# Kernel optimization log

Hardware: AMD Instinct MI355X
Metric: run time of the kernel (lower is better)

Reference implementation:

```python
import jax, jax.numpy as jnp
import numpy as np

TAU = 1.0
NUM_CLASSES = 256
N = 65536
D = 256
EPS = 1e-12  # F.normalize default eps


def _l2_normalize(x):
    norm = jnp.sqrt(jnp.sum(x * x, axis=-1, keepdims=True))
    return x / jnp.maximum(norm, EPS)


def setup_inputs() -> dict:
    key = jax.random.key(0)
    k1, k2, k3 = jax.random.split(key, 3)
    z1 = jax.random.normal(k1, (N, D), dtype=jnp.float32)
    z2 = jax.random.normal(k2, (N, D), dtype=jnp.float32)
    labels = jax.random.randint(k3, (N,), 0, NUM_CLASSES, dtype=jnp.int32)
    return {"z1_features": z1, "z2_features": z2, "labels": labels}


def reference(z1_features, z2_features, labels):
    # labels for both views: [2N]
    labels2 = jnp.concatenate([labels, labels], axis=0)
    z = jnp.concatenate([_l2_normalize(z1_features), _l2_normalize(z2_features)], axis=0)  # [2N, D]

    # per-class mean via segment-sum (replaces the python loop over unique labels)
    sums = jax.ops.segment_sum(z, labels2, num_segments=NUM_CLASSES)            # [C, D]
    counts = jax.ops.segment_sum(jnp.ones((z.shape[0],), z.dtype), labels2,
                                 num_segments=NUM_CLASSES)                       # [C]
    feature_means = sums / jnp.maximum(counts, 1.0)[:, None]                     # [C, D]

    # sim_proto: row-wise dot of each sample with its own class prototype
    # (original wastefully did diag(means_repeated @ z.T))
    proto_per_row = feature_means[labels2]                                        # [2N, D] gather
    sim_proto = jnp.sum(proto_per_row * z, axis=-1) / TAU                         # [2N]

    sim_all = (z @ feature_means.T) / TAU                                         # [2N, C]
    exp_sim = jnp.exp(sim_all - sim_proto[:, None])
    log_prob_pos = sim_proto - jnp.log(jnp.sum(exp_sim, axis=1))
    return -jnp.mean(log_prob_pos)
```

## Files before the change

### kernel.cpp

```cpp
#include <hip/hip_runtime.h>
#include <hip/hip_bf16.h>


constexpr int N_ROWS = 65536;
constexpr int D_DIM  = 256;
constexpr int C_CLS  = 256;
constexpr int TWO_N  = 2 * N_ROWS;
constexpr int BUCKET = 1024;
constexpr float EPS_NORM = 1e-12f;

typedef short          short8   __attribute__((ext_vector_type(8)));
typedef float          f32x16   __attribute__((ext_vector_type(16)));
typedef unsigned short ushort8v __attribute__((ext_vector_type(8)));

constexpr size_t WS_CURSOR = 0;
constexpr size_t WS_LOSSP  = 4096;
constexpr size_t WS_INVN   = 8192;
constexpr size_t WS_ORDER  = WS_INVN + 4ull * TWO_N;
constexpr size_t WS_MEANP  = WS_ORDER + 4ull * C_CLS * BUCKET;
constexpr size_t WS_MEANS  = WS_MEANP + 16ull * C_CLS * D_DIM;

__device__ __forceinline__ void gload_lds16(const void* g, void* l) {
    __builtin_amdgcn_global_load_lds(
        (const __attribute__((address_space(1))) void*)g,
        (__attribute__((address_space(3))) void*)l, 16, 0, 0);
}

__device__ __forceinline__ unsigned short f2bf(float x) {
    __hip_bfloat16 h = __float2bfloat16(x);
    return __builtin_bit_cast(unsigned short, h);
}

__global__ __launch_bounds__(256)
void k_norm(const float* __restrict__ z1, const float* __restrict__ z2,
            float* __restrict__ inv_norm)
{
    const int w = threadIdx.x >> 6, lane = threadIdx.x & 63;
    const int wave = blockIdx.x * 4 + w;
    #pragma unroll 1
    for (int b = 0; b < 4; ++b) {
        int r[4]; float4 v[4]; float s[4];
        #pragma unroll
        for (int j = 0; j < 4; ++j) {
            r[j] = wave + 8192 * (b * 4 + j);
            const float* src = (r[j] < N_ROWS) ? z1 + (size_t)r[j] * D_DIM
                                               : z2 + (size_t)(r[j] - N_ROWS) * D_DIM;
            v[j] = reinterpret_cast<const float4*>(src)[lane];
        }
        #pragma unroll
        for (int j = 0; j < 4; ++j)
            s[j] = v[j].x * v[j].x + v[j].y * v[j].y + v[j].z * v[j].z + v[j].w * v[j].w;
        #pragma unroll
        for (int off = 1; off < 64; off <<= 1) {
            #pragma unroll
            for (int j = 0; j < 4; ++j) s[j] += __shfl_xor(s[j], off, 64);
        }
        if (lane == 0) {
            #pragma unroll
            for (int j = 0; j < 4; ++j)
                inv_norm[r[j]] = 1.0f / fmaxf(sqrtf(s[j]), EPS_NORM);
        }
    }
}

__global__ __launch_bounds__(256)
void k_scatter(const int* __restrict__ labels, int* __restrict__ cursor,
               int* __restrict__ order)
{
    __shared__ int lcur[C_CLS];
    __shared__ int lbase[C_CLS];
    const int t = threadIdx.x;
    lcur[t] = 0;
    __syncthreads();
    const int i0 = blockIdx.x * 2048;
    int lab[8], lpos[8];
    #pragma unroll
    for (int u = 0; u < 8; ++u) {
        const int i = i0 + u * 256 + t;
        lab[u] = labels[(i < N_ROWS) ? i : (i - N_ROWS)];
        lpos[u] = atomicAdd(&lcur[lab[u]], 1);
    }
    __syncthreads();
    if (lcur[t] > 0) lbase[t] = atomicAdd(&cursor[t], lcur[t]);
    __syncthreads();
    #pragma unroll
    for (int u = 0; u < 8; ++u)
        order[lab[u] * BUCKET + lbase[lab[u]] + lpos[u]] = i0 + u * 256 + t;
}

__global__ __launch_bounds__(256)
void k_means(const float* __restrict__ z1, const float* __restrict__ z2,
             const float* __restrict__ inv_norm, const int* __restrict__ cursor,
             const int* __restrict__ order, float* __restrict__ meanp)
{
    __shared__ float4 red4[4][64];
    const int c = blockIdx.x, sgt = blockIdx.y;
    const int lane = threadIdx.x & 63, w = threadIdx.x >> 6;
    const int cnt = cursor[c];
    const int chunk = (cnt + 3) >> 2;
    const int beg = sgt * chunk;
    const int end = min(beg + chunk, cnt);
    const int* ord = order + c * BUCKET;
    float4 acc = {0.f, 0.f, 0.f, 0.f};
    int idx = beg + w;
    for (; idx + 12 < end; idx += 16) {
        int rr[4]; float4 v[4]; float iv[4];
        #pragma unroll
        for (int u = 0; u < 4; ++u) rr[u] = ord[idx + 4 * u];
        #pragma unroll
        for (int u = 0; u < 4; ++u) {
            const float* src = (rr[u] < N_ROWS) ? z1 + (size_t)rr[u] * D_DIM
                                                : z2 + (size_t)(rr[u] - N_ROWS) * D_DIM;
            v[u] = reinterpret_cast<const float4*>(src)[lane];
            iv[u] = inv_norm[rr[u]];
        }
        #pragma unroll
        for (int u = 0; u < 4; ++u) {
            acc.x = fmaf(v[u].x, iv[u], acc.x);
            acc.y = fmaf(v[u].y, iv[u], acc.y);
            acc.z = fmaf(v[u].z, iv[u], acc.z);
            acc.w = fmaf(v[u].w, iv[u], acc.w);
        }
    }
    for (; idx < end; idx += 4) {
        const int r1 = ord[idx];
        const float* src = (r1 < N_ROWS) ? z1 + (size_t)r1 * D_DIM
                                         : z2 + (size_t)(r1 - N_ROWS) * D_DIM;
        const float4 v = reinterpret_cast<const float4*>(src)[lane];
        const float iv = inv_norm[r1];
        acc.x = fmaf(v.x, iv, acc.x); acc.y = fmaf(v.y, iv, acc.y);
        acc.z = fmaf(v.z, iv, acc.z); acc.w = fmaf(v.w, iv, acc.w);
    }
    red4[w][lane] = acc;
    __syncthreads();
    if (w == 0) {
        const float4 a0 = red4[0][lane], a1 = red4[1][lane];
        const float4 a2 = red4[2][lane], a3 = red4[3][lane];
        float4 o;
        o.x = a0.x + a1.x + a2.x + a3.x;  o.y = a0.y + a1.y + a2.y + a3.y;
        o.z = a0.z + a1.z + a2.z + a3.z;  o.w = a0.w + a1.w + a2.w + a3.w;
        *reinterpret_cast<float4*>(meanp + ((size_t)c * 4 + sgt) * D_DIM + 4 * lane) = o;
    }
}

__global__ __launch_bounds__(256)
void k_means2(const float* __restrict__ meanp, const int* __restrict__ cursor,
              __hip_bfloat16* __restrict__ means)
{
    const int tid = blockIdx.x * 256 + threadIdx.x;
    const int c = tid >> 6, l = tid & 63;
    const float invc = 1.0f / fmaxf((float)cursor[c], 1.0f);
    const float4 s0 = *reinterpret_cast<const float4*>(meanp + ((size_t)c * 4 + 0) * D_DIM + 4 * l);
    const float4 s1 = *reinterpret_cast<const float4*>(meanp + ((size_t)c * 4 + 1) * D_DIM + 4 * l);
    const float4 s2 = *reinterpret_cast<const float4*>(meanp + ((size_t)c * 4 + 2) * D_DIM + 4 * l);
    const float4 s3 = *reinterpret_cast<const float4*>(meanp + ((size_t)c * 4 + 3) * D_DIM + 4 * l);
    ushort4 o;
    o.x = f2bf((s0.x + s1.x + s2.x + s3.x) * invc);
    o.y = f2bf((s0.y + s1.y + s2.y + s3.y) * invc);
    o.z = f2bf((s0.z + s1.z + s2.z + s3.z) * invc);
    o.w = f2bf((s0.w + s1.w + s2.w + s3.w) * invc);
    *reinterpret_cast<ushort4*>(means + (size_t)c * D_DIM + 4 * l) = o;
}

__global__ __launch_bounds__(256, 2)
void k_main(const float* __restrict__ z1, const float* __restrict__ z2,
            const float* __restrict__ inv_norm, const int* __restrict__ labels,
            const __hip_bfloat16* __restrict__ means, float* __restrict__ lossp)
{
    __shared__ char smem[65536];
    const int t    = threadIdx.x;
    const int lane = t & 63;
    const int w    = t >> 6;
    const int wr   = w >> 1, wc = w & 1;
    const int l31  = lane & 31;
    const int g16  = (lane >> 5) << 4;
    const int row0 = blockIdx.x * 128;

    const int a_row  = t >> 1;
    const int a_half = t & 1;
    const int grow   = row0 + a_row;
    const float* zsrc = (grow < N_ROWS) ? z1 + (size_t)grow * D_DIM
                                        : z2 + (size_t)(grow - N_ROWS) * D_DIM;
    const float inv_a = inv_norm[grow];
    const int  a_key  = (((a_row & 3) ^ ((a_row >> 3) & 3)) << 4);
    char* const aw0 = smem + a_row * 64 + ((a_half * 32 + 0)  ^ a_key);
    char* const aw1 = smem + a_row * 64 + ((a_half * 32 + 16) ^ a_key);

    const int rkey = (((l31 & 3) ^ ((l31 >> 3) & 3)) << 4);
    f32x16 acc[2][4] = {};
    float4 pre[4];

    auto A_LOAD = [&](int kt) {
        const float4* s = reinterpret_cast<const float4*>(zsrc + kt * 32 + a_half * 16);
        pre[0] = s[0]; pre[1] = s[1]; pre[2] = s[2]; pre[3] = s[3];
    };
    auto A_WRITE = [&](int buf) {
        ushort8v o1, o2;
        o1[0] = f2bf(pre[0].x * inv_a); o1[1] = f2bf(pre[0].y * inv_a);
        o1[2] = f2bf(pre[0].z * inv_a); o1[3] = f2bf(pre[0].w * inv_a);
        o1[4] = f2bf(pre[1].x * inv_a); o1[5] = f2bf(pre[1].y * inv_a);
        o1[6] = f2bf(pre[1].z * inv_a); o1[7] = f2bf(pre[1].w * inv_a);
        o2[0] = f2bf(pre[2].x * inv_a); o2[1] = f2bf(pre[2].y * inv_a);
        o2[2] = f2bf(pre[2].z * inv_a); o2[3] = f2bf(pre[2].w * inv_a);
        o2[4] = f2bf(pre[3].x * inv_a); o2[5] = f2bf(pre[3].y * inv_a);
        o2[6] = f2bf(pre[3].z * inv_a); o2[7] = f2bf(pre[3].w * inv_a);
        *reinterpret_cast<ushort8v*>(aw0 + buf * 8192) = o1;
        *reinterpret_cast<ushort8v*>(aw1 + buf * 8192) = o2;
    };
    auto B_STAGE = [&](int kt, int buf) {
        #pragma unroll
        for (int q = 0; q < 4; ++q) {
            const int g   = q * 256 + t;
            const int c   = g >> 2;
            const int cb  = (g & 3) << 4;
            const int key = (((c & 3) ^ ((c >> 3) & 3)) << 4);
            gload_lds16((const char*)means + (size_t)c * 512 + kt * 64 + (cb ^ key),
                        smem + 16384 + buf * 16384 + q * 4096 + w * 1024);
        }
    };
    auto COMPUTE = [&](int buf) {
        const char* ab = smem + buf * 8192;
        const char* bb = smem + 16384 + buf * 16384;
        #pragma unroll
        for (int ks = 0; ks < 2; ++ks) {
            const int cb = (ks * 32 + g16) ^ rkey;
            const short8 a0 = *reinterpret_cast<const short8*>(ab + (wr * 64 + l31) * 64 + cb);
            const short8 a1 = *reinterpret_cast<const short8*>(ab + (wr * 64 + 32 + l31) * 64 + cb);
            short8 bfr[4];
            #pragma unroll
            for (int n = 0; n < 4; ++n)
                bfr[n] = *reinterpret_cast<const short8*>(bb + (wc * 128 + n * 32 + l31) * 64 + cb);
            #pragma unroll
            for (int n = 0; n < 4; ++n) {
                acc[0][n] = __builtin_amdgcn_mfma_f32_32x32x16_bf16(a0, bfr[n], acc[0][n], 0, 0, 0);
                acc[1][n] = __builtin_amdgcn_mfma_f32_32x32x16_bf16(a1, bfr[n], acc[1][n], 0, 0, 0);
            }
        }
    };

    B_STAGE(0, 0);
    A_LOAD(0);
    A_WRITE(0);
    #pragma unroll
    for (int kt = 0; kt < 8; ++kt) {
        __syncthreads();
        if (kt < 7) { B_STAGE(kt + 1, (kt + 1) & 1); A_LOAD(kt + 1); }
        COMPUTE(kt & 1);
        if (kt < 7) A_WRITE((kt + 1) & 1);
    }
    __syncthreads();

    float* simf = reinterpret_cast<float*>(smem);
    float partial = 0.0f;
    for (int rhalf = 0; rhalf < 2; ++rhalf) {
        if (wr == rhalf) {
            #pragma unroll
            for (int rt = 0; rt < 2; ++rt)
                #pragma unroll
                for (int n = 0; n < 4; ++n)
                    #pragma unroll
                    for (int q = 0; q < 16; ++q) {
                        const int row64 = rt * 32 + (q & 3) + 8 * (q >> 2) + 4 * (lane >> 5);
                        const int col   = wc * 128 + n * 32 + l31;
                        simf[row64 * 256 + col] = acc[rt][n][q];
                    }
        }
        __syncthreads();
        #pragma unroll 1
        for (int i = 0; i < 16; ++i) {
            const int rl    = w * 16 + i;
            const int growr = row0 + rhalf * 64 + rl;
            float s = __expf(simf[rl * 256 + lane])       + __expf(simf[rl * 256 + 64 + lane])
                    + __expf(simf[rl * 256 + 128 + lane]) + __expf(simf[rl * 256 + 192 + lane]);
            #pragma unroll
            for (int off = 32; off; off >>= 1) s += __shfl_down(s, off, 64);
            const int lab = labels[(growr < N_ROWS) ? growr : growr - N_ROWS];
            const float sp = simf[rl * 256 + lab];
            if (lane == 0) partial += 2.0f * sp - logf(s);
        }
        __syncthreads();
    }
    if (lane == 0) simf[w] = partial;
    __syncthreads();
    if (t == 0) lossp[blockIdx.x] = simf[0] + simf[1] + simf[2] + simf[3];
}

__global__ __launch_bounds__(256)
void k_final(const float* __restrict__ lossp, float* __restrict__ out)
{
    __shared__ float red[4];
    const int t = threadIdx.x, lane = t & 63, w = t >> 6;
    float s = lossp[t] + lossp[t + 256] + lossp[t + 512] + lossp[t + 768];
    #pragma unroll
    for (int off = 32; off; off >>= 1) s += __shfl_down(s, off, 64);
    if (lane == 0) red[w] = s;
    __syncthreads();
    if (t == 0) out[0] = -(red[0] + red[1] + red[2] + red[3]) / (float)TWO_N;
}

extern "C" void kernel_launch(void* const* d_in, const int* in_sizes, int n_in,
                              void* d_out, int out_size, void* d_ws, size_t ws_size,
                              hipStream_t stream)
{
    const float* z1     = (const float*)d_in[0];
    const float* z2     = (const float*)d_in[1];
    const int*   labels = (const int*)d_in[2];
    float* out = (float*)d_out;
    char*  ws  = (char*)d_ws;

    int*   cursor   = (int*)  (ws + WS_CURSOR);
    float* lossp    = (float*)(ws + WS_LOSSP);
    float* inv_norm = (float*)(ws + WS_INVN);
    int*   order    = (int*)  (ws + WS_ORDER);
    float* meanp    = (float*)(ws + WS_MEANP);
    __hip_bfloat16* means = (__hip_bfloat16*)(ws + WS_MEANS);

    hipMemsetAsync(ws, 0, 4096, stream);

    hipLaunchKernelGGL(k_norm,    dim3(2048), dim3(256), 0, stream, z1, z2, inv_norm);
    hipLaunchKernelGGL(k_scatter, dim3(64),   dim3(256), 0, stream, labels, cursor, order);
    hipLaunchKernelGGL(k_means,   dim3(256, 4), dim3(256), 0, stream, z1, z2, inv_norm, cursor, order, meanp);
    hipLaunchKernelGGL(k_means2,  dim3(64),   dim3(256), 0, stream, meanp, cursor, means);
    hipLaunchKernelGGL(k_main,    dim3(TWO_N / 128), dim3(256), 0, stream, z1, z2, inv_norm, labels, means, lossp);
    hipLaunchKernelGGL(k_final,   dim3(1),    dim3(256), 0, stream, lossp, out);
}
```

Measured before the change: 236.7 us.

## Materialize normalized bf16 features once and reuse them across means and main kernels

Normalization now writes a bf16 copy of the L2-normalized features, so the class-mean and similarity kernels read half-size data instead of re-reading fp32 inputs and rescaling. The main kernel computes exp-sums and the prototype similarity straight from MFMA accumulators and reduces the loss with an atomic add, which removes the final reduction kernel. This path needs a large workspace and falls back to the old kernels otherwise. Class means are now taken from bf16-rounded features, which slightly changes numerics.

```diff
diff --git a/kernel.cpp b/kernel.cpp
--- a/kernel.cpp
+++ b/kernel.cpp
@@ -13,27 +13,291 @@
 typedef float          f32x16   __attribute__((ext_vector_type(16)));
 typedef unsigned short ushort8v __attribute__((ext_vector_type(8)));
 
-constexpr size_t WS_CURSOR = 0;
-constexpr size_t WS_LOSSP  = 4096;
-constexpr size_t WS_INVN   = 8192;
-constexpr size_t WS_ORDER  = WS_INVN + 4ull * TWO_N;
-constexpr size_t WS_MEANP  = WS_ORDER + 4ull * C_CLS * BUCKET;
-constexpr size_t WS_MEANS  = WS_MEANP + 16ull * C_CLS * D_DIM;
+constexpr size_t CW_CURSOR = 0;
+constexpr size_t CW_MEANP  = 4096;
+constexpr size_t CW_MEANS  = CW_MEANP + 524288;
+constexpr size_t CW_ORDER  = CW_MEANS + 131072;
+constexpr size_t CW_ZNB    = CW_ORDER + 1048576;
+constexpr size_t CW_NEED   = CW_ZNB + 2ull * TWO_N * D_DIM;
+
+constexpr size_t FW_CURSOR = 0;
+constexpr size_t FW_LOSSP  = 4096;
+constexpr size_t FW_INVN   = 8192;
+constexpr size_t FW_ORDER  = FW_INVN + 4ull * TWO_N;
+constexpr size_t FW_MEANP  = FW_ORDER + 4ull * C_CLS * BUCKET;
+constexpr size_t FW_MEANS  = FW_MEANP + 16ull * C_CLS * D_DIM;
 
 __device__ __forceinline__ void gload_lds16(const void* g, void* l) {
     __builtin_amdgcn_global_load_lds(
         (const __attribute__((address_space(1))) void*)g,
         (__attribute__((address_space(3))) void*)l, 16, 0, 0);
 }
-
 __device__ __forceinline__ unsigned short f2bf(float x) {
     __hip_bfloat16 h = __float2bfloat16(x);
     return __builtin_bit_cast(unsigned short, h);
 }
+__device__ __forceinline__ float bf2f(unsigned short u) {
+    return __uint_as_float(((unsigned int)u) << 16);
+}
+
+__global__ __launch_bounds__(256)
+void k_scatter(const int* __restrict__ labels, int* __restrict__ cursor,
+               int* __restrict__ order)
+{
+    __shared__ int lcur[C_CLS];
+    __shared__ int lbase[C_CLS];
+    const int t = threadIdx.x;
+    lcur[t] = 0;
+    __syncthreads();
+    const int i0 = blockIdx.x * 2048;
+    int lab[8], lpos[8];
+    #pragma unroll
+    for (int u = 0; u < 8; ++u) {
+        const int i = i0 + u * 256 + t;
+        lab[u] = labels[(i < N_ROWS) ? i : (i - N_ROWS)];
+        lpos[u] = atomicAdd(&lcur[lab[u]], 1);
+    }
+    __syncthreads();
+    if (lcur[t] > 0) lbase[t] = atomicAdd(&cursor[t], lcur[t]);
+    __syncthreads();
+    #pragma unroll
+    for (int u = 0; u < 8; ++u)
+        order[lab[u] * BUCKET + lbase[lab[u]] + lpos[u]] = i0 + u * 256 + t;
+}
+
 
 __global__ __launch_bounds__(256)
 void k_norm(const float* __restrict__ z1, const float* __restrict__ z2,
-            float* __restrict__ inv_norm)
+            __hip_bfloat16* __restrict__ znb)
+{
+    const int w = threadIdx.x >> 6, lane = threadIdx.x & 63;
+    const int wave = blockIdx.x * 4 + w;
+    #pragma unroll 1
+    for (int b = 0; b < 8; ++b) {
+        const int r0 = wave + 8192 * (2 * b);
+        const int r1 = wave + 8192 * (2 * b + 1);
+        const float* s0p = (r0 < N_ROWS) ? z1 + (size_t)r0 * D_DIM
+                                         : z2 + (size_t)(r0 - N_ROWS) * D_DIM;
+        const float* s1p = (r1 < N_ROWS) ? z1 + (size_t)r1 * D_DIM
+                                         : z2 + (size_t)(r1 - N_ROWS) * D_DIM;
+        const float4 v0 = reinterpret_cast<const float4*>(s0p)[lane];
+        const float4 v1 = reinterpret_cast<const float4*>(s1p)[lane];
+        float s0 = v0.x * v0.x + v0.y * v0.y + v0.z * v0.z + v0.w * v0.w;
+        float s1 = v1.x * v1.x + v1.y * v1.y + v1.z * v1.z + v1.w * v1.w;
+        #pragma unroll
+        for (int off = 1; off < 64; off <<= 1) {
+            s0 += __shfl_xor(s0, off, 64);
+            s1 += __shfl_xor(s1, off, 64);
+        }
+        const float i0 = 1.0f / fmaxf(sqrtf(s0), EPS_NORM);
+        const float i1 = 1.0f / fmaxf(sqrtf(s1), EPS_NORM);
+        ushort4 o0, o1;
+        o0.x = f2bf(v0.x * i0); o0.y = f2bf(v0.y * i0);
+        o0.z = f2bf(v0.z * i0); o0.w = f2bf(v0.w * i0);
+        o1.x = f2bf(v1.x * i1); o1.y = f2bf(v1.y * i1);
+        o1.z = f2bf(v1.z * i1); o1.w = f2bf(v1.w * i1);
+        reinterpret_cast<ushort4*>(znb + (size_t)r0 * D_DIM)[lane] = o0;
+        reinterpret_cast<ushort4*>(znb + (size_t)r1 * D_DIM)[lane] = o1;
+    }
+}
+
+__global__ __launch_bounds__(256)
+void k_meansC(const __hip_bfloat16* __restrict__ znb, const int* __restrict__ cursor,
+              const int* __restrict__ order, float* __restrict__ meanp)
+{
+    __shared__ float red[4][D_DIM];
+    const int c = blockIdx.x, sgt = blockIdx.y;
+    const int t = threadIdx.x, lane = t & 63, w = t >> 6;
+    const int h = lane >> 5, l31 = lane & 31;
+    const int cnt = cursor[c];
+    const int chunk = (cnt + 1) >> 1;
+    const int beg = sgt * chunk;
+    const int end = min(beg + chunk, cnt);
+    const int* ord = order + c * BUCKET;
+
+    float acc[8] = {};
+    int base = beg;
+    for (; base + 32 <= end; base += 32) {
+        #pragma unroll
+        for (int u = 0; u < 4; ++u) {
+            const int r = ord[base + w * 8 + u * 2 + h];
+            const ushort8v v = *reinterpret_cast<const ushort8v*>(
+                znb + (size_t)r * D_DIM + l31 * 8);
+            #pragma unroll
+            for (int j = 0; j < 8; ++j) acc[j] += bf2f(v[j]);
+        }
+    }
+    if (base < end) {
+        #pragma unroll
+        for (int u = 0; u < 4; ++u) {
+            const int ri = base + w * 8 + u * 2 + h;
+            const bool ok = ri < end;
+            const int r = ord[ok ? ri : beg];
+            const ushort8v v = *reinterpret_cast<const ushort8v*>(
+                znb + (size_t)r * D_DIM + l31 * 8);
+            const float sc = ok ? 1.0f : 0.0f;
+            #pragma unroll
+            for (int j = 0; j < 8; ++j) acc[j] += bf2f(v[j]) * sc;
+        }
+    }
+    #pragma unroll
+    for (int j = 0; j < 8; ++j) acc[j] += __shfl_xor(acc[j], 32, 64);
+    if (h == 0) {
+        #pragma unroll
+        for (int j = 0; j < 8; ++j) red[w][l31 * 8 + j] = acc[j];
+    }
+    __syncthreads();
+    const float s = red[0][t] + red[1][t] + red[2][t] + red[3][t];
+    meanp[((size_t)sgt * C_CLS + c) * D_DIM + t] = s;
+}
+
+__global__ __launch_bounds__(256)
+void k_means2C(const float* __restrict__ meanp, const int* __restrict__ cursor,
+               __hip_bfloat16* __restrict__ means)
+{
+    const int tid = blockIdx.x * 256 + threadIdx.x;
+    const int c = tid >> 6, l = tid & 63;
+    const float invc = 1.0f / fmaxf((float)cursor[c], 1.0f);
+    const float4 s0 = *reinterpret_cast<const float4*>(meanp + (size_t)c * D_DIM + 4 * l);
+    const float4 s1 = *reinterpret_cast<const float4*>(meanp + (size_t)(C_CLS + c) * D_DIM + 4 * l);
+    ushort4 o;
+    o.x = f2bf((s0.x + s1.x) * invc);
+    o.y = f2bf((s0.y + s1.y) * invc);
+    o.z = f2bf((s0.z + s1.z) * invc);
+    o.w = f2bf((s0.w + s1.w) * invc);
+    *reinterpret_cast<ushort4*>(means + (size_t)c * D_DIM + 4 * l) = o;
+}
+
+__global__ __launch_bounds__(256, 2)
+void k_mainC(const __hip_bfloat16* __restrict__ znb, const int* __restrict__ labels,
+             const __hip_bfloat16* __restrict__ means, float* __restrict__ out)
+{
+    __shared__ char smem[51712];
+    int*   labs   = reinterpret_cast<int*>(smem + 49152);
+    float* expsum = reinterpret_cast<float*>(smem + 49664);
+    float* proto  = reinterpret_cast<float*>(smem + 50688);
+
+    const int t    = threadIdx.x;
+    const int lane = t & 63;
+    const int w    = t >> 6;
+    const int wr   = w >> 1, wc = w & 1;
+    const int l31  = lane & 31;
+    const int g    = lane >> 5;
+    const int g16  = g << 4;
+    const int row0 = blockIdx.x * 128;
+
+    const char* znbB   = (const char*)znb;
+    const char* meansB = (const char*)means;
+
+    const int skey = ((lane >> 3) & 3) << 4;
+    const int sc   = ((lane & 3) << 4) ^ skey;
+    const int rk   = ((l31 >> 1) & 3) << 4;
+
+    auto A_STAGE = [&](int kt, int buf) {
+        #pragma unroll
+        for (int i = 0; i < 2; ++i) {
+            const int row = w * 32 + i * 16 + (lane >> 2);
+            gload_lds16(znbB + (size_t)(row0 + row) * 512 + kt * 64 + sc,
+                        smem + buf * 8192 + (w * 2 + i) * 1024);
+        }
+    };
+    auto B_STAGE = [&](int kt, int buf) {
+        #pragma unroll
+        for (int j = 0; j < 4; ++j) {
+            const int cls = w * 64 + j * 16 + (lane >> 2);
+            gload_lds16(meansB + (size_t)cls * 512 + kt * 64 + sc,
+                        smem + 16384 + buf * 16384 + (w * 4 + j) * 1024);
+        }
+    };
+
+    f32x16 acc[2][4] = {};
+    auto COMPUTE = [&](int buf) {
+        const char* ab = smem + buf * 8192;
+        const char* bb = smem + 16384 + buf * 16384;
+        #pragma unroll
+        for (int ks = 0; ks < 2; ++ks) {
+            const int co = (ks * 32 + g16) ^ rk;
+            const short8 a0 = *reinterpret_cast<const short8*>(ab + (wr * 64 + l31) * 64 + co);
+            const short8 a1 = *reinterpret_cast<const short8*>(ab + (wr * 64 + 32 + l31) * 64 + co);
+            short8 bfr[4];
+            #pragma unroll
+            for (int n = 0; n < 4; ++n)
+                bfr[n] = *reinterpret_cast<const short8*>(
+                    bb + (wc * 128 + n * 32 + l31) * 64 + co);
+            #pragma unroll
+            for (int n = 0; n < 4; ++n) {
+                acc[0][n] = __builtin_amdgcn_mfma_f32_32x32x16_bf16(a0, bfr[n], acc[0][n], 0, 0, 0);
+                acc[1][n] = __builtin_amdgcn_mfma_f32_32x32x16_bf16(a1, bfr[n], acc[1][n], 0, 0, 0);
+            }
+        }
+    };
+
+    if (t < 128) {
+        const int gr = row0 + t;
+        labs[t] = labels[(gr < N_ROWS) ? gr : gr - N_ROWS];
+    }
+    A_STAGE(0, 0);
+    B_STAGE(0, 0);
+    __syncthreads();
+
+    #pragma unroll
+    for (int kt = 0; kt < 8; ++kt) {
+        if (kt < 7) { A_STAGE(kt + 1, (kt + 1) & 1); B_STAGE(kt + 1, (kt + 1) & 1); }
+        COMPUTE(kt & 1);
+        __syncthreads();
+    }
+
+    float rowsum[2][16];
+    #pragma unroll
+    for (int rt = 0; rt < 2; ++rt)
+        #pragma unroll
+        for (int q = 0; q < 16; ++q) {
+            float s = __expf(acc[rt][0][q]) + __expf(acc[rt][1][q])
+                    + __expf(acc[rt][2][q]) + __expf(acc[rt][3][q]);
+            rowsum[rt][q] = s;
+        }
+    #pragma unroll
+    for (int off = 1; off <= 16; off <<= 1) {
+        #pragma unroll
+        for (int rt = 0; rt < 2; ++rt)
+            #pragma unroll
+            for (int q = 0; q < 16; ++q)
+                rowsum[rt][q] += __shfl_xor(rowsum[rt][q], off, 64);
+    }
+    if (l31 == 0) {
+        #pragma unroll
+        for (int rt = 0; rt < 2; ++rt)
+            #pragma unroll
+            for (int q = 0; q < 16; ++q) {
+                const int r = wr * 64 + rt * 32 + (q & 3) + 8 * (q >> 2) + 4 * g;
+                expsum[r * 2 + wc] = rowsum[rt][q];
+            }
+    }
+    #pragma unroll
+    for (int rt = 0; rt < 2; ++rt)
+        #pragma unroll
+        for (int q = 0; q < 16; ++q) {
+            const int r = wr * 64 + rt * 32 + (q & 3) + 8 * (q >> 2) + 4 * g;
+            const int lab = labs[r];
+            #pragma unroll
+            for (int n = 0; n < 4; ++n)
+                if (lab == wc * 128 + n * 32 + l31) proto[r] = acc[rt][n][q];
+        }
+    __syncthreads();
+
+    if (t < 128) {
+        const float es = expsum[t * 2] + expsum[t * 2 + 1];
+        float lp = 2.0f * proto[t] - __logf(es);
+        #pragma unroll
+        for (int off = 1; off < 64; off <<= 1) lp += __shfl_xor(lp, off, 64);
+        if (lane == 0) atomicAdd(out, -lp * (1.0f / (float)TWO_N));
+    }
+}
+
+
+__global__ __launch_bounds__(256)
+void k_norm_fb(const float* __restrict__ z1, const float* __restrict__ z2,
+               float* __restrict__ inv_norm)
 {
     const int w = threadIdx.x >> 6, lane = threadIdx.x & 63;
     const int wave = blockIdx.x * 4 + w;
@@ -64,34 +328,9 @@
 }
 
 __global__ __launch_bounds__(256)
-void k_scatter(const int* __restrict__ labels, int* __restrict__ cursor,
-               int* __restrict__ order)
-{
-    __shared__ int lcur[C_CLS];
-    __shared__ int lbase[C_CLS];
-    const int t = threadIdx.x;
-    lcur[t] = 0;
-    __syncthreads();
-    const int i0 = blockIdx.x * 2048;
-    int lab[8], lpos[8];
-    #pragma unroll
-    for (int u = 0; u < 8; ++u) {
-        const int i = i0 + u * 256 + t;
-        lab[u] = labels[(i < N_ROWS) ? i : (i - N_ROWS)];
-        lpos[u] = atomicAdd(&lcur[lab[u]], 1);
-    }
-    __syncthreads();
-    if (lcur[t] > 0) lbase[t] = atomicAdd(&cursor[t], lcur[t]);
-    __syncthreads();
-    #pragma unroll
-    for (int u = 0; u < 8; ++u)
-        order[lab[u] * BUCKET + lbase[lab[u]] + lpos[u]] = i0 + u * 256 + t;
-}
-
-__global__ __launch_bounds__(256)
-void k_means(const float* __restrict__ z1, const float* __restrict__ z2,
-             const float* __restrict__ inv_norm, const int* __restrict__ cursor,
-             const int* __restrict__ order, float* __restrict__ meanp)
+void k_means_fb(const float* __restrict__ z1, const float* __restrict__ z2,
+                const float* __restrict__ inv_norm, const int* __restrict__ cursor,
+                const int* __restrict__ order, float* __restrict__ meanp)
 {
     __shared__ float4 red4[4][64];
     const int c = blockIdx.x, sgt = blockIdx.y;
@@ -144,8 +383,8 @@
 }
 
 __global__ __launch_bounds__(256)
-void k_means2(const float* __restrict__ meanp, const int* __restrict__ cursor,
-              __hip_bfloat16* __restrict__ means)
+void k_means2_fb(const float* __restrict__ meanp, const int* __restrict__ cursor,
+                 __hip_bfloat16* __restrict__ means)
 {
     const int tid = blockIdx.x * 256 + threadIdx.x;
     const int c = tid >> 6, l = tid & 63;
@@ -163,9 +402,9 @@
 }
 
 __global__ __launch_bounds__(256, 2)
-void k_main(const float* __restrict__ z1, const float* __restrict__ z2,
-            const float* __restrict__ inv_norm, const int* __restrict__ labels,
-            const __hip_bfloat16* __restrict__ means, float* __restrict__ lossp)
+void k_main_fb(const float* __restrict__ z1, const float* __restrict__ z2,
+               const float* __restrict__ inv_norm, const int* __restrict__ labels,
+               const __hip_bfloat16* __restrict__ means, float* __restrict__ lossp)
 {
     __shared__ char smem[65536];
     const int t    = threadIdx.x;
@@ -210,9 +449,9 @@
     auto B_STAGE = [&](int kt, int buf) {
         #pragma unroll
         for (int q = 0; q < 4; ++q) {
-            const int g   = q * 256 + t;
-            const int c   = g >> 2;
-            const int cb  = (g & 3) << 4;
+            const int gg  = q * 256 + t;
+            const int c   = gg >> 2;
+            const int cb  = (gg & 3) << 4;
             const int key = (((c & 3) ^ ((c >> 3) & 3)) << 4);
             gload_lds16((const char*)means + (size_t)c * 512 + kt * 64 + (cb ^ key),
                         smem + 16384 + buf * 16384 + q * 4096 + w * 1024);
@@ -286,7 +525,7 @@
 }
 
 __global__ __launch_bounds__(256)
-void k_final(const float* __restrict__ lossp, float* __restrict__ out)
+void k_final_fb(const float* __restrict__ lossp, float* __restrict__ out)
 {
     __shared__ float red[4];
     const int t = threadIdx.x, lane = t & 63, w = t >> 6;
@@ -308,19 +547,36 @@
     float* out = (float*)d_out;
     char*  ws  = (char*)d_ws;
 
-    int*   cursor   = (int*)  (ws + WS_CURSOR);
-    float* lossp    = (float*)(ws + WS_LOSSP);
-    float* inv_norm = (float*)(ws + WS_INVN);
-    int*   order    = (int*)  (ws + WS_ORDER);
-    float* meanp    = (float*)(ws + WS_MEANP);
-    __hip_bfloat16* means = (__hip_bfloat16*)(ws + WS_MEANS);
-
-    hipMemsetAsync(ws, 0, 4096, stream);
-
-    hipLaunchKernelGGL(k_norm,    dim3(2048), dim3(256), 0, stream, z1, z2, inv_norm);
-    hipLaunchKernelGGL(k_scatter, dim3(64),   dim3(256), 0, stream, labels, cursor, order);
-    hipLaunchKernelGGL(k_means,   dim3(256, 4), dim3(256), 0, stream, z1, z2, inv_norm, cursor, order, meanp);
-    hipLaunchKernelGGL(k_means2,  dim3(64),   dim3(256), 0, stream, meanp, cursor, means);
-    hipLaunchKernelGGL(k_main,    dim3(TWO_N / 128), dim3(256), 0, stream, z1, z2, inv_norm, labels, means, lossp);
-    hipLaunchKernelGGL(k_final,   dim3(1),    dim3(256), 0, stream, lossp, out);
-}
+    if (ws_size >= CW_NEED) {
+        int*   cursor = (int*)  (ws + CW_CURSOR);
+        float* meanp  = (float*)(ws + CW_MEANP);
+        int*   order  = (int*)  (ws + CW_ORDER);
+        __hip_bfloat16* means = (__hip_bfloat16*)(ws + CW_MEANS);
+        __hip_bfloat16* znb   = (__hip_bfloat16*)(ws + CW_ZNB);
+
+        hipMemsetAsync(ws, 0, 4096, stream);
+        hipMemsetAsync(d_out, 0, sizeof(float), stream);
+
+        hipLaunchKernelGGL(k_norm,    dim3(2048), dim3(256), 0, stream, z1, z2, znb);
+        hipLaunchKernelGGL(k_scatter, dim3(64),   dim3(256), 0, stream, labels, cursor, order);
+        hipLaunchKernelGGL(k_meansC,  dim3(C_CLS, 2), dim3(256), 0, stream, znb, cursor, order, meanp);
+        hipLaunchKernelGGL(k_means2C, dim3(64),   dim3(256), 0, stream, meanp, cursor, means);
+        hipLaunchKernelGGL(k_mainC,   dim3(TWO_N / 128), dim3(256), 0, stream, znb, labels, means, out);
+    } else {
+        int*   cursor   = (int*)  (ws + FW_CURSOR);
+        float* lossp    = (float*)(ws + FW_LOSSP);
+        float* inv_norm = (float*)(ws + FW_INVN);
+        int*   order    = (int*)  (ws + FW_ORDER);
+        float* meanp    = (float*)(ws + FW_MEANP);
+        __hip_bfloat16* means = (__hip_bfloat16*)(ws + FW_MEANS);
+
+        hipMemsetAsync(ws, 0, 4096, stream);
+
+        hipLaunchKernelGGL(k_norm_fb,   dim3(2048), dim3(256), 0, stream, z1, z2, inv_norm);
+        hipLaunchKernelGGL(k_scatter,   dim3(64),   dim3(256), 0, stream, labels, cursor, order);
+        hipLaunchKernelGGL(k_means_fb,  dim3(C_CLS, 4), dim3(256), 0, stream, z1, z2, inv_norm, cursor, order, meanp);
+        hipLaunchKernelGGL(k_means2_fb, dim3(64),   dim3(256), 0, stream, meanp, cursor, means);
+        hipLaunchKernelGGL(k_main_fb,   dim3(TWO_N / 128), dim3(256), 0, stream, z1, z2, inv_norm, labels, means, lossp);
+        hipLaunchKernelGGL(k_final_fb,  dim3(1),    dim3(256), 0, stream, lossp, out);
+    }
+}
```

New measurement: 222.6 us. 5.9% less time.
